# Kernel tuning notes

Hardware: AMD Instinct MI355X
Metric: run time of the kernel (lower is better)

The kernel has to match this reference:

```python
import jax, jax.numpy as jnp
import numpy as np

NUM_HEADS = 16
HIDDEN = 1024
HEAD = HIDDEN // NUM_HEADS

def setup_inputs() -> dict:
    key = jax.random.key(0)
    k1, k2 = jax.random.split(key)
    embeddings = jax.random.normal(k1, (4, 2048, HIDDEN), dtype=jnp.float32)
    w_qkv = jax.random.normal(k2, (HIDDEN, 3 * HIDDEN), dtype=jnp.float32) * (1.0 / np.sqrt(HIDDEN))
    return {"embeddings": embeddings, "w_qkv": w_qkv}

def reference(embeddings, w_qkv):
    b, s, h = embeddings.shape
    # qkv projection (no bias): [b, s, 3*h]
    result = embeddings @ w_qkv
    # split '(qkv nah hdsz)': qkv outermost, then heads, then head dim
    result = result.reshape(b, s, 3, NUM_HEADS, HEAD)
    q = jnp.transpose(result[:, :, 0], (0, 2, 1, 3))  # [b, nah, s, hd]
    k = jnp.transpose(result[:, :, 1], (0, 2, 1, 3))
    v = jnp.transpose(result[:, :, 2], (0, 2, 1, 3))
    # NOTE: original scales by 1/sqrt(hidden_size), not 1/sqrt(head_size)
    scores = jnp.einsum('bnqd,bnkd->bnqk', q, k) / jnp.sqrt(jnp.float32(h))
    probs = jax.nn.softmax(scores, axis=-1)
    ctx = jnp.einsum('bnqk,bnkd->bnqd', probs, v)  # [b, nah, s, hd]
    out = jnp.transpose(ctx, (0, 2, 1, 3)).reshape(b, s, h)
    return out
```

## Files before the change

### kernel.cpp

```cpp
#include <hip/hip_runtime.h>
#include <hip/hip_bf16.h>


typedef __attribute__((ext_vector_type(8))) __bf16 bf16x8;
typedef __attribute__((ext_vector_type(8))) unsigned short u16x8;
typedef __attribute__((ext_vector_type(4))) unsigned short u16x4;
typedef __attribute__((ext_vector_type(4))) float f32x4;

#define B_  4
#define S_  2048
#define H_  1024
#define NH_ 16
#define HD_ 64
#define N3_ 3072
#define M_  (B_*S_)

static __device__ __forceinline__ unsigned short f2bf(float f) {
  __bf16 h = (__bf16)f;
  return __builtin_bit_cast(unsigned short, h);
}

static __device__ __forceinline__ float exp2_fast(float x) {
  float r; asm("v_exp_f32 %0, %1" : "=v"(r) : "v"(x)); return r;
}

static __device__ __forceinline__ void gload_lds16(const unsigned short* g,
                                                   unsigned short* l) {
  __builtin_amdgcn_global_load_lds(
      (const __attribute__((address_space(1))) unsigned int*)g,
      (__attribute__((address_space(3))) unsigned int*)l, 16, 0, 0);
}

__global__ __launch_bounds__(256) void cvt_emb_kernel(
    const float* __restrict__ in, unsigned short* __restrict__ out, int n4) {
  int i = blockIdx.x * blockDim.x + threadIdx.x;
  int stride = gridDim.x * blockDim.x;
  const float4* in4 = (const float4*)in;
  for (; i < n4; i += stride) {
    float4 v = in4[i];
    ushort4 o;
    o.x = f2bf(v.x); o.y = f2bf(v.y); o.z = f2bf(v.z); o.w = f2bf(v.w);
    ((ushort4*)out)[i] = o;
  }
}

__global__ __launch_bounds__(256) void cvt_w_kernel(
    const float* __restrict__ in, unsigned short* __restrict__ out) {
  __shared__ __align__(16) unsigned short tile[64 * 64];
  const int t = threadIdx.x;
  const int n0 = blockIdx.x * 64;
  const int k0 = blockIdx.y * 64;
#pragma unroll
  for (int it = 0; it < 4; ++it) {
    int c = it * 256 + t;
    int row = c >> 4;
    int a = c & 15;
    float4 v = *(const float4*)(in + (size_t)(k0 + row) * N3_ + n0 + a * 4);
    u16x4 o;
    o[0] = f2bf(v.x); o[1] = f2bf(v.y); o[2] = f2bf(v.z); o[3] = f2bf(v.w);
    int swz = (((row & 7) ^ ((row >> 3) & 7)) << 4);
    *(u16x4*)((char*)tile + row * 128 + ((a * 8) ^ swz)) = o;
  }
  __syncthreads();
#pragma unroll
  for (int it = 0; it < 2; ++it) {
    int c = it * 256 + t;
    int n = c >> 3;
    int a = c & 7;
    u16x8 o;
#pragma unroll
    for (int j = 0; j < 8; ++j) {
      int k = a * 8 + j;
      int swz = (((k & 7) ^ ((k >> 3) & 7)) << 4);
      o[j] = *(const unsigned short*)((char*)tile + k * 128 + ((2 * n) ^ swz));
    }
    *(u16x8*)(out + (size_t)(n0 + n) * H_ + k0 + a * 8) = o;
  }
}

__global__ __launch_bounds__(256, 3) void qkv_gemm_kernel(
    const unsigned short* __restrict__ A,
    const unsigned short* __restrict__ BT,
    unsigned short* __restrict__ C) {
  __shared__ __align__(16) unsigned short a_lds[128 * 64];
  __shared__ __align__(16) unsigned short b_lds[128 * 64];
  const int t = threadIdx.x;
  const int lane = t & 63;
  const int w = t >> 6;
  const int wm = w >> 1, wn = w & 1;
  const int m0 = blockIdx.y * 128;
  const int n0 = blockIdx.x * 128;
  const int lr = lane & 15;
  const int lh = lane >> 4;
  const int sr8 = lane >> 3;
  const int sch = (lane & 7) ^ sr8;

  f32x4 acc[4][4];
#pragma unroll
  for (int i = 0; i < 4; i++)
#pragma unroll
    for (int j = 0; j < 4; j++)
#pragma unroll
      for (int r = 0; r < 4; r++) acc[i][j][r] = 0.f;

  const unsigned short* Abase = A + (size_t)(m0 + w * 32 + sr8) * H_ + sch * 8;
  const unsigned short* Bbase = BT + (size_t)(n0 + w * 32 + sr8) * H_ + sch * 8;

  for (int kt = 0; kt < 16; ++kt) {
    __syncthreads();
#pragma unroll
    for (int i = 0; i < 4; ++i) {
      gload_lds16(Abase + (size_t)(i * 8) * H_ + kt * 64,
                  &a_lds[(w * 32 + i * 8) * 64]);
      gload_lds16(Bbase + (size_t)(i * 8) * H_ + kt * 64,
                  &b_lds[(w * 32 + i * 8) * 64]);
    }
    __syncthreads();
#pragma unroll
    for (int kb = 0; kb < 2; ++kb) {
      bf16x8 af[4], bfr[4];
#pragma unroll
      for (int mi = 0; mi < 4; mi++) {
        int row = wm * 64 + mi * 16 + lr;
        int off = (kb * 64 + lh * 16) ^ ((row & 7) << 4);
        af[mi] = *(const bf16x8*)((char*)a_lds + row * 128 + off);
      }
#pragma unroll
      for (int ni = 0; ni < 4; ni++) {
        int row = wn * 64 + ni * 16 + lr;
        int off = (kb * 64 + lh * 16) ^ ((row & 7) << 4);
        bfr[ni] = *(const bf16x8*)((char*)b_lds + row * 128 + off);
      }
#pragma unroll
      for (int mi = 0; mi < 4; mi++)
#pragma unroll
        for (int ni = 0; ni < 4; ni++)
          acc[mi][ni] = __builtin_amdgcn_mfma_f32_16x16x32_bf16(
              af[mi], bfr[ni], acc[mi][ni], 0, 0, 0);
    }
  }
  const float mult = (n0 < H_) ? 0.045084220027780106f : 1.0f;
#pragma unroll
  for (int mi = 0; mi < 4; mi++)
#pragma unroll
    for (int ni = 0; ni < 4; ni++)
#pragma unroll
      for (int rg = 0; rg < 4; rg++) {
        int row = m0 + wm * 64 + mi * 16 + lh * 4 + rg;
        int col = n0 + wn * 64 + ni * 16 + lr;
        C[(size_t)row * N3_ + col] = f2bf(acc[mi][ni][rg] * mult);
      }
}

__global__ __launch_bounds__(256) void vtrans_kernel(
    const unsigned short* __restrict__ qkv, unsigned short* __restrict__ vt) {
  __shared__ __align__(16) unsigned short tile[64 * 64];
  const int t = threadIdx.x;
  const int st = blockIdx.x;
  const int h = blockIdx.y;
  const int b = blockIdx.z;
  const int s0 = st * 64;
#pragma unroll
  for (int it = 0; it < 2; ++it) {
    int c = it * 256 + t;
    int row = c >> 3;
    int a = c & 7;
    u16x8 v = *(const u16x8*)(qkv + (size_t)(b * S_ + s0 + row) * N3_ +
                              2 * H_ + h * HD_ + a * 8);
    int swz = (((row & 7) ^ ((row >> 3) & 7)) << 4);
    *(u16x8*)((char*)tile + row * 128 + ((a * 16) ^ swz)) = v;
  }
  __syncthreads();
#pragma unroll
  for (int it = 0; it < 2; ++it) {
    int c = it * 256 + t;
    int d = c >> 3;
    int a = c & 7;
    u16x8 o;
#pragma unroll
    for (int j = 0; j < 8; ++j) {
      int r = a * 8 + j;
      int swz = (((r & 7) ^ ((r >> 3) & 7)) << 4);
      o[j] = *(const unsigned short*)((char*)tile + r * 128 + ((2 * d) ^ swz));
    }
    int s0a = a * 8, s0b = a * 8 + 4;
    int p_lo = ((s0a >> 5) << 3) | (((s0a >> 2) & 3) << 1) | ((s0a >> 4) & 1);
    int p_hi = ((s0b >> 5) << 3) | (((s0b >> 2) & 3) << 1) | ((s0b >> 4) & 1);
    unsigned short* dst =
        vt + ((size_t)((b * NH_ + h) * HD_) + d) * S_ + s0;
    u16x4 lo = {o[0], o[1], o[2], o[3]};
    u16x4 hi = {o[4], o[5], o[6], o[7]};
    *(u16x4*)(dst + p_lo * 4) = lo;
    *(u16x4*)(dst + p_hi * 4) = hi;
  }
}

__global__ __launch_bounds__(256, 3) void attn_kernel(
    const unsigned short* __restrict__ QKV,
    const unsigned short* __restrict__ VT,
    float* __restrict__ out) {
  __shared__ __align__(16) unsigned short k_lds[64 * 64];
  __shared__ __align__(16) unsigned short vt_lds[64 * 64];
  const int t = threadIdx.x;
  const int lane = t & 63;
  const int w = t >> 6;
  const int lr = lane & 15, lh = lane >> 4;
  const int h = blockIdx.y;
  const int b = blockIdx.z;
  const int qw = blockIdx.x * 128 + w * 32;

  bf16x8 qf[2][2];
#pragma unroll
  for (int qi = 0; qi < 2; ++qi) {
    const unsigned short* qp =
        QKV + (size_t)(b * S_ + qw + qi * 16 + lr) * N3_ + h * HD_ + lh * 8;
    qf[qi][0] = *(const bf16x8*)qp;
    qf[qi][1] = *(const bf16x8*)(qp + 32);
  }

  bf16x8 ones;
#pragma unroll
  for (int j = 0; j < 8; ++j) ones[j] = (lr == 0) ? (__bf16)1.0f : (__bf16)0.0f;

  f32x4 o[2][4], o5[2];
#pragma unroll
  for (int qi = 0; qi < 2; ++qi) {
#pragma unroll
    for (int i = 0; i < 4; i++)
#pragma unroll
      for (int r = 0; r < 4; r++) o[qi][i][r] = 0.f;
#pragma unroll
    for (int r = 0; r < 4; r++) o5[qi][r] = 0.f;
  }
  float mrun[2] = {-3e38f, -3e38f};

  const int row0 = t >> 3, a0 = t & 7;
  const int row1 = (256 + t) >> 3, a1 = t & 7;
  const int dst0 = row0 * 128 + ((a0 * 16) ^ ((row0 & 7) << 4));
  const int dst1 = row1 * 128 + ((a1 * 16) ^ ((row1 & 7) << 4));
  const unsigned short* kbase = QKV + (size_t)(b * S_) * N3_ + H_ + h * HD_;
  const unsigned short* vbase = VT + (size_t)((b * NH_ + h) * HD_) * S_;

  u16x8 gk0 = *(const u16x8*)(kbase + (size_t)row0 * N3_ + a0 * 8);
  u16x8 gk1 = *(const u16x8*)(kbase + (size_t)row1 * N3_ + a1 * 8);
  u16x8 gv0 = *(const u16x8*)(vbase + (size_t)row0 * S_ + a0 * 8);
  u16x8 gv1 = *(const u16x8*)(vbase + (size_t)row1 * S_ + a1 * 8);

  for (int kt = 0; kt < 32; ++kt) {
    __syncthreads();
    *(u16x8*)((char*)k_lds + dst0) = gk0;
    *(u16x8*)((char*)k_lds + dst1) = gk1;
    *(u16x8*)((char*)vt_lds + dst0) = gv0;
    *(u16x8*)((char*)vt_lds + dst1) = gv1;
    __syncthreads();

    {
      int ktn = (kt + 1) & 31;
      const unsigned short* kp = kbase + (size_t)(ktn * 64) * N3_;
      const unsigned short* vp = vbase + ktn * 64;
      gk0 = *(const u16x8*)(kp + (size_t)row0 * N3_ + a0 * 8);
      gk1 = *(const u16x8*)(kp + (size_t)row1 * N3_ + a1 * 8);
      gv0 = *(const u16x8*)(vp + (size_t)row0 * S_ + a0 * 8);
      gv1 = *(const u16x8*)(vp + (size_t)row1 * S_ + a1 * 8);
    }

    f32x4 sacc[2][4];
#pragma unroll
    for (int qi = 0; qi < 2; ++qi)
#pragma unroll
      for (int nt = 0; nt < 4; nt++)
#pragma unroll
        for (int r = 0; r < 4; r++) sacc[qi][nt][r] = 0.f;
#pragma unroll
    for (int nt = 0; nt < 4; ++nt) {
#pragma unroll
      for (int kb = 0; kb < 2; ++kb) {
        int row = nt * 16 + lr;
        bf16x8 kf = *(const bf16x8*)((char*)k_lds + row * 128 +
                                     ((64 * kb + 16 * lh) ^ ((row & 7) << 4)));
        sacc[0][nt] = __builtin_amdgcn_mfma_f32_16x16x32_bf16(kf, qf[0][kb], sacc[0][nt], 0, 0, 0);
        sacc[1][nt] = __builtin_amdgcn_mfma_f32_16x16x32_bf16(kf, qf[1][kb], sacc[1][nt], 0, 0, 0);
      }
    }

    float mx[2];
#pragma unroll
    for (int qi = 0; qi < 2; ++qi) {
      float m = fmaxf(fmaxf(fmaxf(sacc[qi][0][0], sacc[qi][0][1]),
                            fmaxf(sacc[qi][0][2], sacc[qi][0][3])),
                      fmaxf(fmaxf(sacc[qi][1][0], sacc[qi][1][1]),
                            fmaxf(sacc[qi][1][2], sacc[qi][1][3])));
      float m2 = fmaxf(fmaxf(fmaxf(sacc[qi][2][0], sacc[qi][2][1]),
                             fmaxf(sacc[qi][2][2], sacc[qi][2][3])),
                       fmaxf(fmaxf(sacc[qi][3][0], sacc[qi][3][1]),
                             fmaxf(sacc[qi][3][2], sacc[qi][3][3])));
      m = fmaxf(m, m2);
      m = fmaxf(m, __shfl_xor(m, 16, 64));
      m = fmaxf(m, __shfl_xor(m, 32, 64));
      mx[qi] = m;
    }

    bool ok = (mx[0] <= mrun[0] + 8.0f) && (mx[1] <= mrun[1] + 8.0f);
    if (!__all(ok)) {
#pragma unroll
      for (int qi = 0; qi < 2; ++qi) {
        float mn = fmaxf(mrun[qi], mx[qi]);
        float alpha = exp2_fast(mrun[qi] - mn);
        mrun[qi] = mn;
        float al[4];
#pragma unroll
        for (int rg = 0; rg < 4; ++rg) al[rg] = __shfl(alpha, lh * 4 + rg, 64);
#pragma unroll
        for (int dt = 0; dt < 4; ++dt)
#pragma unroll
          for (int rg = 0; rg < 4; ++rg) o[qi][dt][rg] *= al[rg];
#pragma unroll
        for (int rg = 0; rg < 4; ++rg) o5[qi][rg] *= al[rg];
      }
    }

    bf16x8 pa[2][2];
#pragma unroll
    for (int qi = 0; qi < 2; ++qi)
#pragma unroll
      for (int kb = 0; kb < 2; ++kb)
#pragma unroll
        for (int j = 0; j < 8; ++j)
          pa[qi][kb][j] =
              (__bf16)exp2_fast(sacc[qi][2 * kb + (j >> 2)][j & 3] - mrun[qi]);

#pragma unroll
    for (int kb = 0; kb < 2; ++kb) {
#pragma unroll
      for (int dt = 0; dt < 4; ++dt) {
        int row = dt * 16 + lr;
        bf16x8 vb = *(const bf16x8*)((char*)vt_lds + row * 128 +
                                     ((64 * kb + 16 * lh) ^ ((row & 7) << 4)));
        o[0][dt] = __builtin_amdgcn_mfma_f32_16x16x32_bf16(pa[0][kb], vb, o[0][dt], 0, 0, 0);
        o[1][dt] = __builtin_amdgcn_mfma_f32_16x16x32_bf16(pa[1][kb], vb, o[1][dt], 0, 0, 0);
      }
      o5[0] = __builtin_amdgcn_mfma_f32_16x16x32_bf16(pa[0][kb], ones, o5[0], 0, 0, 0);
      o5[1] = __builtin_amdgcn_mfma_f32_16x16x32_bf16(pa[1][kb], ones, o5[1], 0, 0, 0);
    }
  }

#pragma unroll
  for (int qi = 0; qi < 2; ++qi) {
    float inv[4];
#pragma unroll
    for (int rg = 0; rg < 4; ++rg) {
      float ls = __shfl(o5[qi][rg], lh * 16, 64);
      inv[rg] = 1.0f / ls;
    }
#pragma unroll
    for (int dt = 0; dt < 4; ++dt)
#pragma unroll
      for (int rg = 0; rg < 4; ++rg) {
        int qrow = qw + qi * 16 + lh * 4 + rg;
        out[(size_t)(b * S_ + qrow) * H_ + h * HD_ + dt * 16 + lr] =
            o[qi][dt][rg] * inv[rg];
      }
  }
}

extern "C" void kernel_launch(void* const* d_in, const int* in_sizes, int n_in,
                              void* d_out, int out_size, void* d_ws, size_t ws_size,
                              hipStream_t stream) {
  const float* emb = (const float*)d_in[0];
  const float* wqkv = (const float*)d_in[1];
  float* out = (float*)d_out;

  unsigned short* abf = (unsigned short*)d_ws;
  unsigned short* wtb = abf + (size_t)M_ * H_;
  unsigned short* qkv = wtb + (size_t)N3_ * H_;
  unsigned short* vt = abf;

  cvt_emb_kernel<<<dim3(2048), dim3(256), 0, stream>>>(emb, abf, (M_ * H_) / 4);
  cvt_w_kernel<<<dim3(48, 16), dim3(256), 0, stream>>>(wqkv, wtb);
  qkv_gemm_kernel<<<dim3(N3_ / 128, M_ / 128), dim3(256), 0, stream>>>(abf, wtb, qkv);
  vtrans_kernel<<<dim3(32, 16, 4), dim3(256), 0, stream>>>(qkv, vt);
  attn_kernel<<<dim3(16, 16, 4), dim3(256), 0, stream>>>(qkv, vt, out);
}
```

Before: 248.4 us.

## Double-buffer QKV GEMM LDS tiles and remap blocks for XCD locality

The QKV projection GEMM now uses double-buffered LDS with a K-step of 32. The next tile's global-to-LDS loads are issued before the MFMAs on the current tile, and only one barrier runs per iteration, so the load latency should overlap with compute. The grid is flattened to 1D and block IDs are swizzled so that consecutive blocks on the same XCD share rows and columns, which should improve L2 reuse. In exchange the loop runs twice as many iterations with half the MFMA work per barrier, and the LDS layout and XOR swizzle are rewritten for 64-byte rows.

```diff
diff --git a/kernel.cpp b/kernel.cpp
--- a/kernel.cpp
+++ b/kernel.cpp
@@ -82,18 +82,33 @@
     const unsigned short* __restrict__ A,
     const unsigned short* __restrict__ BT,
     unsigned short* __restrict__ C) {
-  __shared__ __align__(16) unsigned short a_lds[128 * 64];
-  __shared__ __align__(16) unsigned short b_lds[128 * 64];
+  __shared__ __align__(16) unsigned short lds[2][2][128 * 32];
   const int t = threadIdx.x;
   const int lane = t & 63;
   const int w = t >> 6;
   const int wm = w >> 1, wn = w & 1;
-  const int m0 = blockIdx.y * 128;
-  const int n0 = blockIdx.x * 128;
+  const int wg = blockIdx.x;
+  const int swz = (wg & 7) * 192 + (wg >> 3);
+  const int n0 = (swz % 24) * 128;
+  const int m0 = (swz / 24) * 128;
   const int lr = lane & 15;
   const int lh = lane >> 4;
-  const int sr8 = lane >> 3;
-  const int sch = (lane & 7) ^ sr8;
+  const int ach = (lh ^ (lr & 3)) * 16;
+
+  const int srow = w * 16 + (lane >> 2);
+  const int sch = (lane & 3) ^ ((lane >> 2) & 3);
+  const unsigned short* As = A + (size_t)(m0 + srow) * H_ + sch * 8;
+  const unsigned short* Bs = BT + (size_t)(n0 + srow) * H_ + sch * 8;
+
+#define STAGE(SB, KT)                                                        \
+  do {                                                                       \
+    gload_lds16(As + (size_t)(KT) * 32, &lds[SB][0][(w * 16) * 32]);         \
+    gload_lds16(As + 64 * (size_t)H_ + (size_t)(KT) * 32,                    \
+                &lds[SB][0][(64 + w * 16) * 32]);                            \
+    gload_lds16(Bs + (size_t)(KT) * 32, &lds[SB][1][(w * 16) * 32]);         \
+    gload_lds16(Bs + 64 * (size_t)H_ + (size_t)(KT) * 32,                    \
+                &lds[SB][1][(64 + w * 16) * 32]);                            \
+  } while (0)
 
   f32x4 acc[4][4];
 #pragma unroll
@@ -103,42 +118,31 @@
 #pragma unroll
       for (int r = 0; r < 4; r++) acc[i][j][r] = 0.f;
 
-  const unsigned short* Abase = A + (size_t)(m0 + w * 32 + sr8) * H_ + sch * 8;
-  const unsigned short* Bbase = BT + (size_t)(n0 + w * 32 + sr8) * H_ + sch * 8;
-
-  for (int kt = 0; kt < 16; ++kt) {
+  STAGE(0, 0);
+  __syncthreads();
+
+  for (int kt = 0; kt < 32; ++kt) {
+    const int cur = kt & 1;
+    if (kt < 31) STAGE(cur ^ 1, kt + 1);
+    bf16x8 af[4], bfr[4];
+#pragma unroll
+    for (int mi = 0; mi < 4; ++mi)
+      af[mi] = *(const bf16x8*)((const char*)&lds[cur][0][0] +
+                                (wm * 64 + mi * 16 + lr) * 64 + ach);
+#pragma unroll
+    for (int ni = 0; ni < 4; ++ni)
+      bfr[ni] = *(const bf16x8*)((const char*)&lds[cur][1][0] +
+                                 (wn * 64 + ni * 16 + lr) * 64 + ach);
+#pragma unroll
+    for (int mi = 0; mi < 4; ++mi)
+#pragma unroll
+      for (int ni = 0; ni < 4; ++ni)
+        acc[mi][ni] = __builtin_amdgcn_mfma_f32_16x16x32_bf16(
+            af[mi], bfr[ni], acc[mi][ni], 0, 0, 0);
     __syncthreads();
-#pragma unroll
-    for (int i = 0; i < 4; ++i) {
-      gload_lds16(Abase + (size_t)(i * 8) * H_ + kt * 64,
-                  &a_lds[(w * 32 + i * 8) * 64]);
-      gload_lds16(Bbase + (size_t)(i * 8) * H_ + kt * 64,
-                  &b_lds[(w * 32 + i * 8) * 64]);
-    }
-    __syncthreads();
-#pragma unroll
-    for (int kb = 0; kb < 2; ++kb) {
-      bf16x8 af[4], bfr[4];
-#pragma unroll
-      for (int mi = 0; mi < 4; mi++) {
-        int row = wm * 64 + mi * 16 + lr;
-        int off = (kb * 64 + lh * 16) ^ ((row & 7) << 4);
-        af[mi] = *(const bf16x8*)((char*)a_lds + row * 128 + off);
-      }
-#pragma unroll
-      for (int ni = 0; ni < 4; ni++) {
-        int row = wn * 64 + ni * 16 + lr;
-        int off = (kb * 64 + lh * 16) ^ ((row & 7) << 4);
-        bfr[ni] = *(const bf16x8*)((char*)b_lds + row * 128 + off);
-      }
-#pragma unroll
-      for (int mi = 0; mi < 4; mi++)
-#pragma unroll
-        for (int ni = 0; ni < 4; ni++)
-          acc[mi][ni] = __builtin_amdgcn_mfma_f32_16x16x32_bf16(
-              af[mi], bfr[ni], acc[mi][ni], 0, 0, 0);
-    }
-  }
+  }
+#undef STAGE
+
   const float mult = (n0 < H_) ? 0.045084220027780106f : 1.0f;
 #pragma unroll
   for (int mi = 0; mi < 4; mi++)
@@ -377,7 +381,7 @@
 
   cvt_emb_kernel<<<dim3(2048), dim3(256), 0, stream>>>(emb, abf, (M_ * H_) / 4);
   cvt_w_kernel<<<dim3(48, 16), dim3(256), 0, stream>>>(wqkv, wtb);
-  qkv_gemm_kernel<<<dim3(N3_ / 128, M_ / 128), dim3(256), 0, stream>>>(abf, wtb, qkv);
+  qkv_gemm_kernel<<<dim3(1536), dim3(256), 0, stream>>>(abf, wtb, qkv);
   vtrans_kernel<<<dim3(32, 16, 4), dim3(256), 0, stream>>>(qkv, vt);
   attn_kernel<<<dim3(16, 16, 4), dim3(256), 0, stream>>>(qkv, vt, out);
 }
```

Measured after the change: 250.5 us. Within noise of the previous version (+0.8%).
